# Performance work log

Hardware: AMD Instinct MI355X
Metric: run time of the kernel (lower is better)

Reference implementation:

```python
import jax, jax.numpy as jnp
import numpy as np

DIM = 512
N_HEADS = 8
HEAD_DIM = DIM // N_HEADS


def rope_pos(T, head_dim, dtype=jnp.float32):
    inv_freq = 1.0 / (10000.0 ** (jnp.arange(0, head_dim, 2, dtype=jnp.float32) / head_dim))
    t = jnp.arange(T, dtype=jnp.float32)
    freqs = jnp.einsum('i,j->ij', t, inv_freq)            # [T, head_dim/2]
    return jnp.concatenate([freqs, freqs], axis=-1).astype(dtype)  # [T, head_dim]


def rotate_half(x):
    x1, x2 = jnp.split(x, 2, axis=-1)
    return jnp.concatenate([-x2, x1], axis=-1)


def apply_rope(pos, t):
    # pos: [T, hd] -> broadcast to [1,1,T,hd]; t: [B,H,T,hd]
    pos = pos[None, None, :, :]
    return t * jnp.cos(pos) + rotate_half(t) * jnp.sin(pos)


def setup_inputs() -> dict:
    key = jax.random.key(0)
    ks = jax.random.split(key, 6)
    B, T = 4, 2048
    x = jax.random.normal(ks[0], (B, T, DIM), dtype=jnp.float32)
    mask = jnp.zeros((B, T), dtype=jnp.float32)  # additive mask
    s = 1.0 / np.sqrt(DIM)
    qkv_w = jax.random.normal(ks[1], (3 * DIM, DIM), dtype=jnp.float32) * s
    qkv_b = jnp.zeros((3 * DIM,), dtype=jnp.float32)
    proj_w = jax.random.normal(ks[2], (DIM, DIM), dtype=jnp.float32) * s
    proj_b = jnp.zeros((DIM,), dtype=jnp.float32)
    return {"x": x, "mask": mask, "qkv_w": qkv_w, "qkv_b": qkv_b,
            "proj_w": proj_w, "proj_b": proj_b}


def reference(x, mask, qkv_w, qkv_b, proj_w, proj_b):
    B, T, C = x.shape
    qkv = x @ qkv_w.T + qkv_b                       # [B,T,3C]
    qkv = qkv.reshape(B, T, 3, N_HEADS, HEAD_DIM)
    q, k, v = qkv[:, :, 0], qkv[:, :, 1], qkv[:, :, 2]  # [B,T,H,hd]
    q = q.transpose(0, 2, 1, 3)                     # [B,H,T,hd]
    k = k.transpose(0, 2, 1, 3)
    v = v.transpose(0, 2, 1, 3)
    pos = rope_pos(T, HEAD_DIM, x.dtype)
    q = apply_rope(pos, q)
    k = apply_rope(pos, k)
    scores = jnp.einsum('bhqd,bhkd->bhqk', q, k) * (1.0 / np.sqrt(HEAD_DIM))
    scores = scores + mask[:, None, None, :]        # 2D mask -> [B,1,1,T]
    probs = jax.nn.softmax(scores.astype(jnp.float32), axis=-1).astype(x.dtype)
    # dropout is identity in eval mode
    out = jnp.einsum('bhqk,bhkd->bhqd', probs, v)   # [B,H,T,hd]
    out = out.transpose(0, 2, 1, 3).reshape(B, T, C)
    return out @ proj_w.T + proj_b
```

## Files before the change

### kernel.cpp

```cpp
#include <hip/hip_runtime.h>
#include <math.h>


typedef __attribute__((ext_vector_type(8))) short bf16x8;
typedef __attribute__((ext_vector_type(4))) float floatx4;

#define LOG2E 1.44269504088896f

__device__ __forceinline__ unsigned short f2bf(float f) {
  unsigned int u = __float_as_uint(f);
  u += 0x7fffu + ((u >> 16) & 1u);
  return (unsigned short)(u >> 16);
}

__device__ __forceinline__ void gld_lds16(unsigned short* lds, const unsigned short* g) {
  __builtin_amdgcn_global_load_lds(
      (const __attribute__((address_space(1))) unsigned int*)g,
      (__attribute__((address_space(3))) unsigned int*)lds, 16, 0, 0);
}

__global__ __launch_bounds__(256) void prep_kernel(
    const float* __restrict__ x, const float* __restrict__ wq, const float* __restrict__ wp,
    unsigned short* __restrict__ xb, unsigned short* __restrict__ wqb,
    unsigned short* __restrict__ wpb, float* __restrict__ cosT, float* __restrict__ sinT) {
  int i = blockIdx.x * 256 + threadIdx.x;
  if (i < 4194304) {
    xb[i] = f2bf(x[i]);
  } else if (i < 4980736) {
    int j = i - 4194304; wqb[j] = f2bf(wq[j]);
  } else if (i < 5242880) {
    int j = i - 4980736; wpb[j] = f2bf(wp[j]);
  } else if (i < 5308416) {
    int j = i - 5242880;
    int t = j >> 5, f = j & 31;
    double fr = (double)t * pow(10000.0, -(double)f / 32.0);
    cosT[j] = (float)cos(fr);
    sinT[j] = (float)sin(fr);
  }
}

__global__ __launch_bounds__(256) void qkv_kernel(
    const unsigned short* __restrict__ xb, const unsigned short* __restrict__ wqb,
    const float* __restrict__ qkv_b, const float* __restrict__ cosT,
    const float* __restrict__ sinT, unsigned short* __restrict__ Qb,
    unsigned short* __restrict__ Kb, unsigned short* __restrict__ Vtb) {
  __shared__ __align__(16) unsigned short As[128 * 32];
  __shared__ __align__(16) unsigned short Bs[128 * 32];
  const int tid = threadIdx.x;
  const int wave = tid >> 6, lane = tid & 63, ln = lane & 15, quad = lane >> 4;
  const int m0 = blockIdx.x * 128, n0 = blockIdx.y * 128;
  const int wr = (wave >> 1) * 64, wc = (wave & 1) * 64;

  floatx4 acc[4][4];
#pragma unroll
  for (int i = 0; i < 4; ++i)
#pragma unroll
    for (int j = 0; j < 4; ++j) acc[i][j] = (floatx4){0.f, 0.f, 0.f, 0.f};

  const int c0 = tid, c1 = tid + 256;
  const int ar0 = c0 >> 2, ak0 = (c0 & 3) * 8;
  const int ar1 = c1 >> 2, ak1 = (c1 & 3) * 8;

  for (int k0 = 0; k0 < 512; k0 += 32) {
    __syncthreads();
    gld_lds16(As + c0 * 8, xb + (size_t)(m0 + ar0) * 512 + k0 + ak0);
    gld_lds16(As + c1 * 8, xb + (size_t)(m0 + ar1) * 512 + k0 + ak1);
    gld_lds16(Bs + c0 * 8, wqb + (size_t)(n0 + ar0) * 512 + k0 + ak0);
    gld_lds16(Bs + c1 * 8, wqb + (size_t)(n0 + ar1) * 512 + k0 + ak1);
    __syncthreads();
    bf16x8 af[4], bfb[4];
#pragma unroll
    for (int mi = 0; mi < 4; ++mi)
      af[mi] = *(const bf16x8*)(As + (wr + mi * 16 + ln) * 32 + quad * 8);
#pragma unroll
    for (int ni = 0; ni < 4; ++ni)
      bfb[ni] = *(const bf16x8*)(Bs + (wc + ni * 16 + ln) * 32 + quad * 8);
#pragma unroll
    for (int mi = 0; mi < 4; ++mi)
#pragma unroll
      for (int ni = 0; ni < 4; ++ni)
        acc[mi][ni] = __builtin_amdgcn_mfma_f32_16x16x32_bf16(af[mi], bfb[ni], acc[mi][ni], 0, 0, 0);
  }

  const int colbase = n0 + wc;
  const int mat = colbase >> 9;
  const int h = (colbase & 511) >> 6;
  float bias[4];
#pragma unroll
  for (int ni = 0; ni < 4; ++ni) bias[ni] = qkv_b[colbase + ni * 16 + ln];

  if (mat == 2) {
#pragma unroll
    for (int mi = 0; mi < 4; ++mi) {
      int row0 = m0 + wr + mi * 16 + quad * 4;
      int bidx = row0 >> 11, t = row0 & 2047;
#pragma unroll
      for (int ni = 0; ni < 4; ++ni) {
        int d = ni * 16 + ln;
        ushort4 pk;
        pk.x = f2bf(acc[mi][ni][0] + bias[ni]);
        pk.y = f2bf(acc[mi][ni][1] + bias[ni]);
        pk.z = f2bf(acc[mi][ni][2] + bias[ni]);
        pk.w = f2bf(acc[mi][ni][3] + bias[ni]);
        *(ushort4*)(Vtb + ((size_t)(bidx * 8 + h) * 64 + d) * 2048 + t) = pk;
      }
    }
  } else {
    unsigned short* dst = (mat == 0) ? Qb : Kb;
    const float sc = (mat == 0) ? 0.125f * LOG2E : 1.0f;
#pragma unroll
    for (int mi = 0; mi < 4; ++mi) {
#pragma unroll
      for (int r = 0; r < 4; ++r) {
        int row = m0 + wr + mi * 16 + quad * 4 + r;
        int bidx = row >> 11, t = row & 2047;
        const float* cr = cosT + t * 32;
        const float* sr = sinT + t * 32;
        size_t obase = ((size_t)(bidx * 8 + h) * 2048 + t) * 64;
#pragma unroll
        for (int ni = 0; ni < 2; ++ni) {
          int dlo = ni * 16 + ln;
          float cv = cr[dlo], sv = sr[dlo];
          float xlo = acc[mi][ni][r] + bias[ni];
          float xhi = acc[mi][ni + 2][r] + bias[ni + 2];
          dst[obase + dlo]      = f2bf((xlo * cv - xhi * sv) * sc);
          dst[obase + dlo + 32] = f2bf((xhi * cv + xlo * sv) * sc);
        }
      }
    }
  }
}

__global__ __launch_bounds__(256) void attn_kernel(
    const unsigned short* __restrict__ Qb, const unsigned short* __restrict__ Kb,
    const unsigned short* __restrict__ Vtb, const float* __restrict__ mask,
    unsigned short* __restrict__ attnb) {
  __shared__ __align__(16) unsigned short Ks[64 * 72];
  __shared__ __align__(16) unsigned short Vs[64 * 72];
  __shared__ __align__(16) unsigned short Ps[128 * 72];

  const int tid = threadIdx.x;
  const int wave = tid >> 6, lane = tid & 63, ln = lane & 15, quad = lane >> 4;
  const int bh = blockIdx.y;
  const int b = bh >> 3, h = bh & 7;
  const int wq0 = blockIdx.x * 128 + wave * 32;

  const unsigned short* Qhead = Qb + (size_t)bh * 2048 * 64;
  const unsigned short* Khead = Kb + (size_t)bh * 2048 * 64;
  const unsigned short* Vhead = Vtb + (size_t)bh * 64 * 2048;

  bf16x8 qf[2][2];
#pragma unroll
  for (int ni2 = 0; ni2 < 2; ++ni2)
#pragma unroll
    for (int ks = 0; ks < 2; ++ks)
      qf[ni2][ks] = *(const bf16x8*)(Qhead + (size_t)(wq0 + ni2 * 16 + ln) * 64 + ks * 32 + quad * 8);

  floatx4 o[4][2];
#pragma unroll
  for (int mi2 = 0; mi2 < 4; ++mi2)
#pragma unroll
    for (int ni2 = 0; ni2 < 2; ++ni2) o[mi2][ni2] = (floatx4){0.f, 0.f, 0.f, 0.f};
  float mrun[2] = {-INFINITY, -INFINITY};
  float lrun[2] = {0.f, 0.f};

  const int srow = tid >> 3, soff = (tid & 7) * 8;
  uint4 kpre0 = *(const uint4*)(Khead + (size_t)srow * 64 + soff);
  uint4 kpre1 = *(const uint4*)(Khead + (size_t)(srow + 32) * 64 + soff);
  uint4 vpre0 = *(const uint4*)(Vhead + (size_t)srow * 2048 + soff);
  uint4 vpre1 = *(const uint4*)(Vhead + (size_t)(srow + 32) * 2048 + soff);

  for (int k0 = 0; k0 < 2048; k0 += 64) {
    __syncthreads();
    *(uint4*)(Ks + srow * 72 + soff) = kpre0;
    *(uint4*)(Ks + (srow + 32) * 72 + soff) = kpre1;
    *(uint4*)(Vs + srow * 72 + soff) = vpre0;
    *(uint4*)(Vs + (srow + 32) * 72 + soff) = vpre1;
    __syncthreads();
    if (k0 + 64 < 2048) {
      kpre0 = *(const uint4*)(Khead + (size_t)(k0 + 64 + srow) * 64 + soff);
      kpre1 = *(const uint4*)(Khead + (size_t)(k0 + 64 + srow + 32) * 64 + soff);
      vpre0 = *(const uint4*)(Vhead + (size_t)srow * 2048 + k0 + 64 + soff);
      vpre1 = *(const uint4*)(Vhead + (size_t)(srow + 32) * 2048 + k0 + 64 + soff);
    }

    floatx4 sm[4][2];
#pragma unroll
    for (int mi = 0; mi < 4; ++mi) {
      bf16x8 kf0 = *(const bf16x8*)(Ks + (mi * 16 + ln) * 72 + quad * 8);
      bf16x8 kf1 = *(const bf16x8*)(Ks + (mi * 16 + ln) * 72 + 32 + quad * 8);
#pragma unroll
      for (int ni2 = 0; ni2 < 2; ++ni2) {
        floatx4 a = (floatx4){0.f, 0.f, 0.f, 0.f};
        a = __builtin_amdgcn_mfma_f32_16x16x32_bf16(kf0, qf[ni2][0], a, 0, 0, 0);
        a = __builtin_amdgcn_mfma_f32_16x16x32_bf16(kf1, qf[ni2][1], a, 0, 0, 0);
        sm[mi][ni2] = a;
      }
    }
#pragma unroll
    for (int mi = 0; mi < 4; ++mi) {
      float4 mv = *(const float4*)(mask + b * 2048 + k0 + mi * 16 + quad * 4);
      float m0v = mv.x * LOG2E, m1v = mv.y * LOG2E, m2v = mv.z * LOG2E, m3v = mv.w * LOG2E;
#pragma unroll
      for (int ni2 = 0; ni2 < 2; ++ni2) {
        sm[mi][ni2][0] += m0v; sm[mi][ni2][1] += m1v;
        sm[mi][ni2][2] += m2v; sm[mi][ni2][3] += m3v;
      }
    }
    float alpha[2];
#pragma unroll
    for (int ni2 = 0; ni2 < 2; ++ni2) {
      float vmax = sm[0][ni2][0];
#pragma unroll
      for (int mi = 0; mi < 4; ++mi)
#pragma unroll
        for (int r = 0; r < 4; ++r) vmax = fmaxf(vmax, sm[mi][ni2][r]);
      vmax = fmaxf(vmax, __shfl_xor(vmax, 16));
      vmax = fmaxf(vmax, __shfl_xor(vmax, 32));
      float nm = fmaxf(mrun[ni2], vmax);
      alpha[ni2] = exp2f(mrun[ni2] - nm);
      mrun[ni2] = nm;
    }
    float psum[2] = {0.f, 0.f};
#pragma unroll
    for (int mi = 0; mi < 4; ++mi)
#pragma unroll
      for (int ni2 = 0; ni2 < 2; ++ni2)
#pragma unroll
        for (int r = 0; r < 4; ++r) {
          float p = exp2f(sm[mi][ni2][r] - mrun[ni2]);
          sm[mi][ni2][r] = p;
          psum[ni2] += p;
        }
#pragma unroll
    for (int ni2 = 0; ni2 < 2; ++ni2) {
      float s = psum[ni2];
      s += __shfl_xor(s, 16);
      s += __shfl_xor(s, 32);
      lrun[ni2] = lrun[ni2] * alpha[ni2] + s;
    }
#pragma unroll
    for (int mi2 = 0; mi2 < 4; ++mi2)
#pragma unroll
      for (int ni2 = 0; ni2 < 2; ++ni2) {
        o[mi2][ni2][0] *= alpha[ni2]; o[mi2][ni2][1] *= alpha[ni2];
        o[mi2][ni2][2] *= alpha[ni2]; o[mi2][ni2][3] *= alpha[ni2];
      }
#pragma unroll
    for (int mi = 0; mi < 4; ++mi)
#pragma unroll
      for (int ni2 = 0; ni2 < 2; ++ni2) {
        ushort4 pk;
        pk.x = f2bf(sm[mi][ni2][0]); pk.y = f2bf(sm[mi][ni2][1]);
        pk.z = f2bf(sm[mi][ni2][2]); pk.w = f2bf(sm[mi][ni2][3]);
        *(ushort4*)(Ps + (wq0 - blockIdx.x * 128 + ni2 * 16 + ln) * 72 + mi * 16 + quad * 4) = pk;
      }
#pragma unroll
    for (int ks = 0; ks < 2; ++ks) {
      bf16x8 pb[2];
#pragma unroll
      for (int ni2 = 0; ni2 < 2; ++ni2)
        pb[ni2] = *(const bf16x8*)(Ps + (wave * 32 + ni2 * 16 + ln) * 72 + ks * 32 + quad * 8);
#pragma unroll
      for (int mi2 = 0; mi2 < 4; ++mi2) {
        bf16x8 vf = *(const bf16x8*)(Vs + (mi2 * 16 + ln) * 72 + ks * 32 + quad * 8);
#pragma unroll
        for (int ni2 = 0; ni2 < 2; ++ni2)
          o[mi2][ni2] = __builtin_amdgcn_mfma_f32_16x16x32_bf16(vf, pb[ni2], o[mi2][ni2], 0, 0, 0);
      }
    }
  }

#pragma unroll
  for (int ni2 = 0; ni2 < 2; ++ni2) {
    float inv = 1.f / lrun[ni2];
    int t = wq0 + ni2 * 16 + ln;
    size_t base = ((size_t)b * 2048 + t) * 512 + h * 64;
#pragma unroll
    for (int mi2 = 0; mi2 < 4; ++mi2) {
      ushort4 pk;
      pk.x = f2bf(o[mi2][ni2][0] * inv); pk.y = f2bf(o[mi2][ni2][1] * inv);
      pk.z = f2bf(o[mi2][ni2][2] * inv); pk.w = f2bf(o[mi2][ni2][3] * inv);
      *(ushort4*)(attnb + base + mi2 * 16 + quad * 4) = pk;
    }
  }
}

__global__ __launch_bounds__(256) void proj_kernel(
    const unsigned short* __restrict__ ab, const unsigned short* __restrict__ wpb,
    const float* __restrict__ proj_b, float* __restrict__ out) {
  __shared__ __align__(16) unsigned short As[128 * 32];
  __shared__ __align__(16) unsigned short Bs[128 * 32];
  const int tid = threadIdx.x;
  const int wave = tid >> 6, lane = tid & 63, ln = lane & 15, quad = lane >> 4;
  const int m0 = blockIdx.x * 128, n0 = blockIdx.y * 128;
  const int wr = (wave >> 1) * 64, wc = (wave & 1) * 64;

  floatx4 acc[4][4];
#pragma unroll
  for (int i = 0; i < 4; ++i)
#pragma unroll
    for (int j = 0; j < 4; ++j) acc[i][j] = (floatx4){0.f, 0.f, 0.f, 0.f};

  const int c0 = tid, c1 = tid + 256;
  const int ar0 = c0 >> 2, ak0 = (c0 & 3) * 8;
  const int ar1 = c1 >> 2, ak1 = (c1 & 3) * 8;

  for (int k0 = 0; k0 < 512; k0 += 32) {
    __syncthreads();
    gld_lds16(As + c0 * 8, ab + (size_t)(m0 + ar0) * 512 + k0 + ak0);
    gld_lds16(As + c1 * 8, ab + (size_t)(m0 + ar1) * 512 + k0 + ak1);
    gld_lds16(Bs + c0 * 8, wpb + (size_t)(n0 + ar0) * 512 + k0 + ak0);
    gld_lds16(Bs + c1 * 8, wpb + (size_t)(n0 + ar1) * 512 + k0 + ak1);
    __syncthreads();
    bf16x8 af[4], bfb[4];
#pragma unroll
    for (int mi = 0; mi < 4; ++mi)
      af[mi] = *(const bf16x8*)(As + (wr + mi * 16 + ln) * 32 + quad * 8);
#pragma unroll
    for (int ni = 0; ni < 4; ++ni)
      bfb[ni] = *(const bf16x8*)(Bs + (wc + ni * 16 + ln) * 32 + quad * 8);
#pragma unroll
    for (int mi = 0; mi < 4; ++mi)
#pragma unroll
      for (int ni = 0; ni < 4; ++ni)
        acc[mi][ni] = __builtin_amdgcn_mfma_f32_16x16x32_bf16(af[mi], bfb[ni], acc[mi][ni], 0, 0, 0);
  }

#pragma unroll
  for (int mi = 0; mi < 4; ++mi)
#pragma unroll
    for (int ni = 0; ni < 4; ++ni) {
      int col = n0 + wc + ni * 16 + ln;
      float pb = proj_b[col];
#pragma unroll
      for (int r = 0; r < 4; ++r) {
        int row = m0 + wr + mi * 16 + quad * 4 + r;
        out[(size_t)row * 512 + col] = acc[mi][ni][r] + pb;
      }
    }
}

extern "C" void kernel_launch(void* const* d_in, const int* in_sizes, int n_in,
                              void* d_out, int out_size, void* d_ws, size_t ws_size,
                              hipStream_t stream) {
  const float* x      = (const float*)d_in[0];
  const float* mask   = (const float*)d_in[1];
  const float* qkv_w  = (const float*)d_in[2];
  const float* qkv_b  = (const float*)d_in[3];
  const float* proj_w = (const float*)d_in[4];
  const float* proj_b = (const float*)d_in[5];
  float* out = (float*)d_out;

  char* ws = (char*)d_ws;
  unsigned short* xb   = (unsigned short*)(ws);
  unsigned short* wqb  = (unsigned short*)(ws + 8388608);
  unsigned short* wpb  = (unsigned short*)(ws + 9961472);
  float* cosT          = (float*)(ws + 10485760);
  float* sinT          = (float*)(ws + 10747904);
  unsigned short* Qb   = (unsigned short*)(ws + 11010048);
  unsigned short* Kb   = (unsigned short*)(ws + 19398656);
  unsigned short* Vtb  = (unsigned short*)(ws + 27787264);
  unsigned short* attnb= (unsigned short*)(ws + 36175872);

  prep_kernel<<<20736, 256, 0, stream>>>(x, qkv_w, proj_w, xb, wqb, wpb, cosT, sinT);
  dim3 g1(64, 12);
  qkv_kernel<<<g1, 256, 0, stream>>>(xb, wqb, qkv_b, cosT, sinT, Qb, Kb, Vtb);
  dim3 g2(16, 32);
  attn_kernel<<<g2, 256, 0, stream>>>(Qb, Kb, Vtb, mask, attnb);
  dim3 g3(64, 4);
  proj_kernel<<<g3, 256, 0, stream>>>(attnb, wpb, proj_b, out);
}
```

Baseline: 215.2 us.

## Split attention work across 8 waves with XOR-swizzled LDS and lazy rescale

The attention kernel now launches 512 threads per block, and each wave handles 16 query rows instead of 32. This halves per-wave registers and doubles the waves available to hide latency. The padded LDS tiles are replaced by an XOR-swizzled 64-wide layout to avoid bank conflicts without padding. The online-softmax rescale is skipped when no row max increases, and bf16 packing uses the hardware v_cvt_pk_bf16_f32 instruction. In exchange, each K/V tile is reused by fewer query rows per wave, and the larger block adds barrier cost.

```diff
diff --git a/kernel.cpp b/kernel.cpp
--- a/kernel.cpp
+++ b/kernel.cpp
@@ -11,6 +11,12 @@
   unsigned int u = __float_as_uint(f);
   u += 0x7fffu + ((u >> 16) & 1u);
   return (unsigned short)(u >> 16);
+}
+
+__device__ __forceinline__ unsigned int cvtpk_bf16(float a, float b) {
+  unsigned int r;
+  asm("v_cvt_pk_bf16_f32 %0, %1, %2" : "=v"(r) : "v"(a), "v"(b));
+  return r;
 }
 
 __device__ __forceinline__ void gld_lds16(unsigned short* lds, const unsigned short* g) {
@@ -131,157 +137,127 @@
   }
 }
 
-__global__ __launch_bounds__(256) void attn_kernel(
+__global__ __launch_bounds__(512) void attn_kernel(
     const unsigned short* __restrict__ Qb, const unsigned short* __restrict__ Kb,
     const unsigned short* __restrict__ Vtb, const float* __restrict__ mask,
     unsigned short* __restrict__ attnb) {
-  __shared__ __align__(16) unsigned short Ks[64 * 72];
-  __shared__ __align__(16) unsigned short Vs[64 * 72];
-  __shared__ __align__(16) unsigned short Ps[128 * 72];
+  __shared__ __align__(16) unsigned short Ks[64 * 64];
+  __shared__ __align__(16) unsigned short Vs[64 * 64];
+  __shared__ __align__(16) unsigned short Ps[128 * 64];
 
   const int tid = threadIdx.x;
   const int wave = tid >> 6, lane = tid & 63, ln = lane & 15, quad = lane >> 4;
+  const int swz = (ln & 7) << 3;
   const int bh = blockIdx.y;
   const int b = bh >> 3, h = bh & 7;
-  const int wq0 = blockIdx.x * 128 + wave * 32;
+  const int q0 = blockIdx.x * 128;
+  const int wq = wave * 16;
 
   const unsigned short* Qhead = Qb + (size_t)bh * 2048 * 64;
   const unsigned short* Khead = Kb + (size_t)bh * 2048 * 64;
   const unsigned short* Vhead = Vtb + (size_t)bh * 64 * 2048;
 
-  bf16x8 qf[2][2];
-#pragma unroll
-  for (int ni2 = 0; ni2 < 2; ++ni2)
-#pragma unroll
-    for (int ks = 0; ks < 2; ++ks)
-      qf[ni2][ks] = *(const bf16x8*)(Qhead + (size_t)(wq0 + ni2 * 16 + ln) * 64 + ks * 32 + quad * 8);
-
-  floatx4 o[4][2];
-#pragma unroll
-  for (int mi2 = 0; mi2 < 4; ++mi2)
-#pragma unroll
-    for (int ni2 = 0; ni2 < 2; ++ni2) o[mi2][ni2] = (floatx4){0.f, 0.f, 0.f, 0.f};
-  float mrun[2] = {-INFINITY, -INFINITY};
-  float lrun[2] = {0.f, 0.f};
-
-  const int srow = tid >> 3, soff = (tid & 7) * 8;
-  uint4 kpre0 = *(const uint4*)(Khead + (size_t)srow * 64 + soff);
-  uint4 kpre1 = *(const uint4*)(Khead + (size_t)(srow + 32) * 64 + soff);
-  uint4 vpre0 = *(const uint4*)(Vhead + (size_t)srow * 2048 + soff);
-  uint4 vpre1 = *(const uint4*)(Vhead + (size_t)(srow + 32) * 2048 + soff);
+  bf16x8 qf[2];
+#pragma unroll
+  for (int ks = 0; ks < 2; ++ks)
+    qf[ks] = *(const bf16x8*)(Qhead + (size_t)(q0 + wq + ln) * 64 + ks * 32 + quad * 8);
+
+  floatx4 o[4];
+#pragma unroll
+  for (int mi2 = 0; mi2 < 4; ++mi2) o[mi2] = (floatx4){0.f, 0.f, 0.f, 0.f};
+  float mrun = -INFINITY;
+  float lrun = 0.f;
+
+  const int srow = tid >> 3;
+  const int scol = (tid & 7) * 8;
+  const int sdst = srow * 64 + (scol ^ ((srow & 7) << 3));
+  uint4 kpre = *(const uint4*)(Khead + (size_t)srow * 64 + scol);
+  uint4 vpre = *(const uint4*)(Vhead + (size_t)srow * 2048 + scol);
 
   for (int k0 = 0; k0 < 2048; k0 += 64) {
     __syncthreads();
-    *(uint4*)(Ks + srow * 72 + soff) = kpre0;
-    *(uint4*)(Ks + (srow + 32) * 72 + soff) = kpre1;
-    *(uint4*)(Vs + srow * 72 + soff) = vpre0;
-    *(uint4*)(Vs + (srow + 32) * 72 + soff) = vpre1;
+    *(uint4*)(Ks + sdst) = kpre;
+    *(uint4*)(Vs + sdst) = vpre;
     __syncthreads();
     if (k0 + 64 < 2048) {
-      kpre0 = *(const uint4*)(Khead + (size_t)(k0 + 64 + srow) * 64 + soff);
-      kpre1 = *(const uint4*)(Khead + (size_t)(k0 + 64 + srow + 32) * 64 + soff);
-      vpre0 = *(const uint4*)(Vhead + (size_t)srow * 2048 + k0 + 64 + soff);
-      vpre1 = *(const uint4*)(Vhead + (size_t)(srow + 32) * 2048 + k0 + 64 + soff);
-    }
-
-    floatx4 sm[4][2];
-#pragma unroll
-    for (int mi = 0; mi < 4; ++mi) {
-      bf16x8 kf0 = *(const bf16x8*)(Ks + (mi * 16 + ln) * 72 + quad * 8);
-      bf16x8 kf1 = *(const bf16x8*)(Ks + (mi * 16 + ln) * 72 + 32 + quad * 8);
-#pragma unroll
-      for (int ni2 = 0; ni2 < 2; ++ni2) {
-        floatx4 a = (floatx4){0.f, 0.f, 0.f, 0.f};
-        a = __builtin_amdgcn_mfma_f32_16x16x32_bf16(kf0, qf[ni2][0], a, 0, 0, 0);
-        a = __builtin_amdgcn_mfma_f32_16x16x32_bf16(kf1, qf[ni2][1], a, 0, 0, 0);
-        sm[mi][ni2] = a;
-      }
+      kpre = *(const uint4*)(Khead + (size_t)(k0 + 64 + srow) * 64 + scol);
+      vpre = *(const uint4*)(Vhead + (size_t)srow * 2048 + k0 + 64 + scol);
+    }
+
+    floatx4 sm[4];
+#pragma unroll
+    for (int mi = 0; mi < 4; ++mi) {
+      bf16x8 kf0 = *(const bf16x8*)(Ks + (mi * 16 + ln) * 64 + ((quad * 8) ^ swz));
+      bf16x8 kf1 = *(const bf16x8*)(Ks + (mi * 16 + ln) * 64 + ((32 + quad * 8) ^ swz));
+      floatx4 a = (floatx4){0.f, 0.f, 0.f, 0.f};
+      a = __builtin_amdgcn_mfma_f32_16x16x32_bf16(kf0, qf[0], a, 0, 0, 0);
+      a = __builtin_amdgcn_mfma_f32_16x16x32_bf16(kf1, qf[1], a, 0, 0, 0);
+      sm[mi] = a;
     }
 #pragma unroll
     for (int mi = 0; mi < 4; ++mi) {
       float4 mv = *(const float4*)(mask + b * 2048 + k0 + mi * 16 + quad * 4);
-      float m0v = mv.x * LOG2E, m1v = mv.y * LOG2E, m2v = mv.z * LOG2E, m3v = mv.w * LOG2E;
-#pragma unroll
-      for (int ni2 = 0; ni2 < 2; ++ni2) {
-        sm[mi][ni2][0] += m0v; sm[mi][ni2][1] += m1v;
-        sm[mi][ni2][2] += m2v; sm[mi][ni2][3] += m3v;
-      }
-    }
-    float alpha[2];
-#pragma unroll
-    for (int ni2 = 0; ni2 < 2; ++ni2) {
-      float vmax = sm[0][ni2][0];
-#pragma unroll
-      for (int mi = 0; mi < 4; ++mi)
-#pragma unroll
-        for (int r = 0; r < 4; ++r) vmax = fmaxf(vmax, sm[mi][ni2][r]);
-      vmax = fmaxf(vmax, __shfl_xor(vmax, 16));
-      vmax = fmaxf(vmax, __shfl_xor(vmax, 32));
-      float nm = fmaxf(mrun[ni2], vmax);
-      alpha[ni2] = exp2f(mrun[ni2] - nm);
-      mrun[ni2] = nm;
-    }
-    float psum[2] = {0.f, 0.f};
-#pragma unroll
-    for (int mi = 0; mi < 4; ++mi)
-#pragma unroll
-      for (int ni2 = 0; ni2 < 2; ++ni2)
-#pragma unroll
-        for (int r = 0; r < 4; ++r) {
-          float p = exp2f(sm[mi][ni2][r] - mrun[ni2]);
-          sm[mi][ni2][r] = p;
-          psum[ni2] += p;
-        }
-#pragma unroll
-    for (int ni2 = 0; ni2 < 2; ++ni2) {
-      float s = psum[ni2];
-      s += __shfl_xor(s, 16);
-      s += __shfl_xor(s, 32);
-      lrun[ni2] = lrun[ni2] * alpha[ni2] + s;
-    }
-#pragma unroll
-    for (int mi2 = 0; mi2 < 4; ++mi2)
-#pragma unroll
-      for (int ni2 = 0; ni2 < 2; ++ni2) {
-        o[mi2][ni2][0] *= alpha[ni2]; o[mi2][ni2][1] *= alpha[ni2];
-        o[mi2][ni2][2] *= alpha[ni2]; o[mi2][ni2][3] *= alpha[ni2];
-      }
-#pragma unroll
-    for (int mi = 0; mi < 4; ++mi)
-#pragma unroll
-      for (int ni2 = 0; ni2 < 2; ++ni2) {
-        ushort4 pk;
-        pk.x = f2bf(sm[mi][ni2][0]); pk.y = f2bf(sm[mi][ni2][1]);
-        pk.z = f2bf(sm[mi][ni2][2]); pk.w = f2bf(sm[mi][ni2][3]);
-        *(ushort4*)(Ps + (wq0 - blockIdx.x * 128 + ni2 * 16 + ln) * 72 + mi * 16 + quad * 4) = pk;
-      }
+      sm[mi][0] += mv.x * LOG2E; sm[mi][1] += mv.y * LOG2E;
+      sm[mi][2] += mv.z * LOG2E; sm[mi][3] += mv.w * LOG2E;
+    }
+    float vmax = fmaxf(fmaxf(sm[0][0], sm[0][1]), fmaxf(sm[0][2], sm[0][3]));
+#pragma unroll
+    for (int mi = 1; mi < 4; ++mi)
+      vmax = fmaxf(vmax, fmaxf(fmaxf(sm[mi][0], sm[mi][1]), fmaxf(sm[mi][2], sm[mi][3])));
+    vmax = fmaxf(vmax, __shfl_xor(vmax, 16));
+    vmax = fmaxf(vmax, __shfl_xor(vmax, 32));
+    if (__any(vmax > mrun)) {
+      float nm = fmaxf(mrun, vmax);
+      float alpha = exp2f(mrun - nm);
+      mrun = nm;
+      lrun *= alpha;
+#pragma unroll
+      for (int mi2 = 0; mi2 < 4; ++mi2) {
+        o[mi2][0] *= alpha; o[mi2][1] *= alpha;
+        o[mi2][2] *= alpha; o[mi2][3] *= alpha;
+      }
+    }
+    float psum = 0.f;
+#pragma unroll
+    for (int mi = 0; mi < 4; ++mi)
+#pragma unroll
+      for (int r = 0; r < 4; ++r) {
+        float p = exp2f(sm[mi][r] - mrun);
+        sm[mi][r] = p;
+        psum += p;
+      }
+    psum += __shfl_xor(psum, 16);
+    psum += __shfl_xor(psum, 32);
+    lrun += psum;
+
+#pragma unroll
+    for (int mi = 0; mi < 4; ++mi) {
+      uint2 pk;
+      pk.x = cvtpk_bf16(sm[mi][0], sm[mi][1]);
+      pk.y = cvtpk_bf16(sm[mi][2], sm[mi][3]);
+      *(uint2*)(Ps + (wq + ln) * 64 + ((mi * 16 + quad * 4) ^ swz)) = pk;
+    }
 #pragma unroll
     for (int ks = 0; ks < 2; ++ks) {
-      bf16x8 pb[2];
-#pragma unroll
-      for (int ni2 = 0; ni2 < 2; ++ni2)
-        pb[ni2] = *(const bf16x8*)(Ps + (wave * 32 + ni2 * 16 + ln) * 72 + ks * 32 + quad * 8);
+      bf16x8 pb = *(const bf16x8*)(Ps + (wq + ln) * 64 + ((ks * 32 + quad * 8) ^ swz));
 #pragma unroll
       for (int mi2 = 0; mi2 < 4; ++mi2) {
-        bf16x8 vf = *(const bf16x8*)(Vs + (mi2 * 16 + ln) * 72 + ks * 32 + quad * 8);
-#pragma unroll
-        for (int ni2 = 0; ni2 < 2; ++ni2)
-          o[mi2][ni2] = __builtin_amdgcn_mfma_f32_16x16x32_bf16(vf, pb[ni2], o[mi2][ni2], 0, 0, 0);
-      }
-    }
-  }
-
-#pragma unroll
-  for (int ni2 = 0; ni2 < 2; ++ni2) {
-    float inv = 1.f / lrun[ni2];
-    int t = wq0 + ni2 * 16 + ln;
+        bf16x8 vf = *(const bf16x8*)(Vs + (mi2 * 16 + ln) * 64 + ((ks * 32 + quad * 8) ^ swz));
+        o[mi2] = __builtin_amdgcn_mfma_f32_16x16x32_bf16(vf, pb, o[mi2], 0, 0, 0);
+      }
+    }
+  }
+
+  {
+    float inv = 1.f / lrun;
+    int t = q0 + wq + ln;
     size_t base = ((size_t)b * 2048 + t) * 512 + h * 64;
 #pragma unroll
     for (int mi2 = 0; mi2 < 4; ++mi2) {
-      ushort4 pk;
-      pk.x = f2bf(o[mi2][ni2][0] * inv); pk.y = f2bf(o[mi2][ni2][1] * inv);
-      pk.z = f2bf(o[mi2][ni2][2] * inv); pk.w = f2bf(o[mi2][ni2][3] * inv);
-      *(ushort4*)(attnb + base + mi2 * 16 + quad * 4) = pk;
+      uint2 pk;
+      pk.x = cvtpk_bf16(o[mi2][0] * inv, o[mi2][1] * inv);
+      pk.y = cvtpk_bf16(o[mi2][2] * inv, o[mi2][3] * inv);
+      *(uint2*)(attnb + base + mi2 * 16 + quad * 4) = pk;
     }
   }
 }
@@ -367,7 +343,7 @@
   dim3 g1(64, 12);
   qkv_kernel<<<g1, 256, 0, stream>>>(xb, wqb, qkv_b, cosT, sinT, Qb, Kb, Vtb);
   dim3 g2(16, 32);
-  attn_kernel<<<g2, 256, 0, stream>>>(Qb, Kb, Vtb, mask, attnb);
+  attn_kernel<<<g2, 512, 0, stream>>>(Qb, Kb, Vtb, mask, attnb);
   dim3 g3(64, 4);
   proj_kernel<<<g3, 256, 0, stream>>>(attnb, wpb, proj_b, out);
 }
```

After: 198.2 us. 1.09x faster.
